# Kernel tuning notes

Measured on AMD Instinct MI355X. Metric: run time of the kernel, lower is better.

Reference implementation:

```python
import jax, jax.numpy as jnp
import numpy as np
from jax import lax

GN_GROUPS = 32
EPS = 1e-5


def conv_gn_silu(x, W, b, scale, bias, stride, padding):
    # Conv2d (OIHW weights, NCHW data) -> GroupNorm(32) -> SiLU
    y = lax.conv_general_dilated(
        x, W, (stride, stride), [(padding, padding), (padding, padding)],
        dimension_numbers=("NCHW", "OIHW", "NCHW")) + b[None, :, None, None]
    B, C, H, Wd = y.shape
    yr = y.reshape(B, GN_GROUPS, C // GN_GROUPS, H, Wd)
    mu = yr.mean(axis=(2, 3, 4), keepdims=True)
    var = yr.var(axis=(2, 3, 4), keepdims=True)
    yn = ((yr - mu) * lax.rsqrt(var + EPS)).reshape(B, C, H, Wd)
    yn = yn * scale[None, :, None, None] + bias[None, :, None, None]
    return yn * jax.nn.sigmoid(yn)  # SiLU


def setup_inputs() -> dict:
    key = jax.random.key(0)
    ks = jax.random.split(key, 8)
    C = 256
    B, H, W = 8, 64, 64
    f = lambda k, shp, s: jax.random.normal(k, shp, dtype=jnp.float32) * s
    return {
        "x": f(ks[0], (B, C, H, W), 1.0),
        "y": f(ks[1], (B, C, H, W), 1.0),
        "Wq": f(ks[2], (C, C, 3, 3), 0.02),
        "bq": jnp.zeros((C,), jnp.float32),
        "gq_scale": jnp.ones((C,), jnp.float32),
        "gq_bias": jnp.zeros((C,), jnp.float32),
        "Wk": f(ks[3], (C, C, 2, 2), 0.02),
        "bk": jnp.zeros((C,), jnp.float32),
        "gk_scale": jnp.ones((C,), jnp.float32),
        "gk_bias": jnp.zeros((C,), jnp.float32),
        "Wv": f(ks[4], (C, C, 2, 2), 0.02),
        "bv": jnp.zeros((C,), jnp.float32),
        "gv_scale": jnp.ones((C,), jnp.float32),
        "gv_bias": jnp.zeros((C,), jnp.float32),
        "gamma": f(ks[5], (1,), 1.0),
    }


def reference(x, y, Wq, bq, gq_scale, gq_bias, Wk, bk, gk_scale, gk_bias,
              Wv, bv, gv_scale, gv_bias, gamma):
    B, C, H, W = x.shape
    sr = 2
    Cq = C  # in_dim // factor, factor=1
    q = conv_gn_silu(x, Wq, bq, gq_scale, gq_bias, stride=1, padding=1)   # [B,Cq,H,W]
    k = conv_gn_silu(y, Wk, bk, gk_scale, gk_bias, stride=sr, padding=0)  # [B,Cq,H/sr,W/sr]
    v = conv_gn_silu(y, Wv, bv, gv_scale, gv_bias, stride=sr, padding=0)  # [B,C,H/sr,W/sr]
    N = H * W
    M = (H // sr) * (W // sr)
    q = q.reshape(B, Cq, N)   # proj_query (pre-permute)
    k = k.reshape(B, Cq, M)   # proj_key
    v = v.reshape(B, C, M)    # proj_value
    scale = 1.0 / np.sqrt(Cq).astype(np.float32)
    energy = jnp.einsum("bcn,bcm->bnm", q, k) * scale       # [B,N,M]
    attn = jax.nn.softmax(energy, axis=-1)                   # softmax over keys
    out = jnp.einsum("bcm,bnm->bcn", v, attn).reshape(B, C, H, W)
    return gamma * out
```

## Files before the change

kernel.cpp:

```cpp
#include <hip/hip_runtime.h>
#include <hip/hip_bf16.h>
#include <math.h>

#define B_ 8
#define C_ 256
#define H_ 64
#define W_ 64
#define N_ 4096
#define M_ 1024
#define HW_ 4096

typedef __attribute__((ext_vector_type(8))) short short8;
typedef __attribute__((ext_vector_type(4))) float f32x4;

__device__ __forceinline__ unsigned short f2bf(float x) {
    unsigned u = __float_as_uint(x);
    u += 0x7fffu + ((u >> 16) & 1u);
    return (unsigned short)(u >> 16);
}
__device__ __forceinline__ float bf2f(unsigned short h) {
    return __uint_as_float(((unsigned)h) << 16);
}

__device__ __forceinline__ void gl_lds16(const unsigned short* g, unsigned short* l) {
    __builtin_amdgcn_global_load_lds(
        (const __attribute__((address_space(1))) unsigned int*)g,
        (__attribute__((address_space(3))) unsigned int*)l, 16, 0, 0);
}

__global__ __launch_bounds__(256) void split_w_tap(
    const float* __restrict__ Wq, unsigned short* __restrict__ wtH,
    unsigned short* __restrict__ wtL)
{
    int co = blockIdx.x, ci = threadIdx.x;
    const float* wp = Wq + ((size_t)co * 256 + ci) * 9;
    #pragma unroll
    for (int tap = 0; tap < 9; ++tap) {
        float v = wp[tap];
        unsigned short h = f2bf(v), l = f2bf(v - bf2f(h));
        size_t o = ((size_t)tap << 16) + ((size_t)co << 8) + ci;
        wtH[o] = h; wtL[o] = l;
    }
}

__global__ __launch_bounds__(256) void split_w2(
    const float* __restrict__ Wsrc, unsigned short* __restrict__ wH,
    unsigned short* __restrict__ wL)
{
    int co = blockIdx.x, ci = threadIdx.x;
    const float* wp = Wsrc + ((size_t)co * 256 + ci) * 4;
    #pragma unroll
    for (int tap = 0; tap < 4; ++tap) {
        float v = wp[tap];
        unsigned short h = f2bf(v), l = f2bf(v - bf2f(h));
        size_t o = ((size_t)tap << 16) + ((size_t)co << 8) + ci;
        wH[o] = h; wL[o] = l;
    }
}

__global__ __launch_bounds__(256) void split_x_pad(
    const float* __restrict__ x, unsigned short* __restrict__ xpH,
    unsigned short* __restrict__ xpL)
{
    __shared__ float tile[64][65];
    int blk = blockIdx.x;
    int b = blk >> 6, h = blk & 63;
    int t = threadIdx.x;
    const float* xb = x + ((size_t)b << 20) + (size_t)h * 64;
    size_t obase = (((size_t)b * 4356) + (size_t)(h + 1) * 66 + 1) * 256;
    unsigned short* oH = xpH + obase;
    unsigned short* oL = xpL + obase;
    for (int cc = 0; cc < 256; cc += 64) {
        int wi = t & 63, cq = t >> 6;
        #pragma unroll
        for (int r = 0; r < 16; ++r) {
            int cl = cq * 16 + r;
            tile[cl][wi] = xb[((size_t)(cc + cl)) * 4096 + wi];
        }
        __syncthreads();
        int cl = t & 63, wq = t >> 6;
        #pragma unroll
        for (int r = 0; r < 16; ++r) {
            int wwi = wq * 16 + r;
            float v = tile[cl][wwi];
            unsigned short hh = f2bf(v), lo = f2bf(v - bf2f(hh));
            size_t o = (size_t)wwi * 256 + cc + cl;
            oH[o] = hh; oL[o] = lo;
        }
        __syncthreads();
    }
}

__global__ __launch_bounds__(256) void split_y_t(
    const float* __restrict__ y, unsigned short* __restrict__ yTh,
    unsigned short* __restrict__ yTl, int b0)
{
    __shared__ float tile[64][65];
    int blk = blockIdx.x;
    int bl = blk >> 6, h = blk & 63;
    int t = threadIdx.x;
    const float* yb = y + ((size_t)(b0 + bl) << 20) + (size_t)h * 64;
    size_t obase = (((size_t)bl << 12) + (size_t)h * 64) * 256;
    unsigned short* oH = yTh + obase;
    unsigned short* oL = yTl + obase;
    for (int cc = 0; cc < 256; cc += 64) {
        int wi = t & 63, cq = t >> 6;
        #pragma unroll
        for (int r = 0; r < 16; ++r) {
            int cl = cq * 16 + r;
            tile[cl][wi] = yb[((size_t)(cc + cl)) * 4096 + wi];
        }
        __syncthreads();
        int cl = t & 63, wq = t >> 6;
        #pragma unroll
        for (int r = 0; r < 16; ++r) {
            int wwi = wq * 16 + r;
            float v = tile[cl][wwi];
            unsigned short hh = f2bf(v), lo = f2bf(v - bf2f(hh));
            size_t o = (size_t)wwi * 256 + cc + cl;
            oH[o] = hh; oL[o] = lo;
        }
        __syncthreads();
    }
}

__global__ __launch_bounds__(256, 2) void conv3x3_mfma(
    const unsigned short* __restrict__ xpH, const unsigned short* __restrict__ xpL,
    const unsigned short* __restrict__ wtH, const unsigned short* __restrict__ wtL,
    const float* __restrict__ bq,
    unsigned short* __restrict__ qH, unsigned short* __restrict__ qL)
{
    __shared__ __align__(16) unsigned short bldsH[272 * 32];
    __shared__ __align__(16) unsigned short bldsL[272 * 32];
    __shared__ __align__(16) unsigned short aldsH[2][128 * 32];
    __shared__ __align__(16) unsigned short aldsL[2][128 * 32];

    int blk = blockIdx.x;
    int bat = blk & 7;
    int rest = blk >> 3;
    int cot = rest & 1;
    int pxt = rest >> 1;
    int t = threadIdx.x;
    int w = t >> 6;
    int wco = w >> 1, wpx = w & 1;
    int lane = t & 63;
    int ll = lane & 15, qd = lane >> 4;
    const int h0 = pxt * 2;
    const int co0b = cot * 128;

    const unsigned short* xpHb = xpH + (size_t)bat * 4356 * 256;
    const unsigned short* xpLb = xpL + (size_t)bat * 4356 * 256;

    f32x4 acc[4][4];
    #pragma unroll
    for (int i = 0; i < 4; ++i)
        #pragma unroll
        for (int j = 0; j < 4; ++j) acc[i][j] = (f32x4){0.f, 0.f, 0.f, 0.f};

    int buf = 0;
    for (int chunk = 0; chunk < 8; ++chunk) {
        const int ci0 = chunk * 32;
        for (int j = w; j < 34; j += 4) {
            int half = (j >= 17);
            int jj = half ? j - 17 : j;
            int gid = jj * 64 + lane;
            int cell = gid >> 2;
            int g = gid & 3;
            int cellc = cell < 264 ? cell : 263;
            int dr = cellc / 66;
            int cc = cellc - dr * 66;
            const unsigned short* src = (half ? xpLb : xpHb)
                + (((size_t)(h0 + dr) * 66 + cc) << 8) + ci0
                + ((g ^ (cellc & 3)) << 3);
            unsigned short* dst = (half ? bldsL : bldsH) + jj * 512;
            gl_lds16(src, dst);
        }
        for (int j = w; j < 16; j += 4) {
            int half = j >> 3;
            int jj = j & 7;
            int gid = jj * 64 + lane;
            int co = gid >> 2;
            int g = gid & 3;
            const unsigned short* src = (half ? wtL : wtH)
                + (((size_t)(co0b + co)) << 8) + ci0 + ((g ^ (co & 3)) << 3);
            unsigned short* dst = (half ? aldsL[buf] : aldsH[buf]) + jj * 512;
            gl_lds16(src, dst);
        }
        __syncthreads();

        for (int tap = 0; tap < 9; ++tap) {
            if (tap < 8) {
                const int aoff = (tap + 1) << 16;
                for (int j = w; j < 16; j += 4) {
                    int half = j >> 3;
                    int jj = j & 7;
                    int gid = jj * 64 + lane;
                    int co = gid >> 2;
                    int g = gid & 3;
                    const unsigned short* src = (half ? wtL : wtH)
                        + aoff + (((size_t)(co0b + co)) << 8) + ci0
                        + ((g ^ (co & 3)) << 3);
                    unsigned short* dst = (half ? aldsL[buf ^ 1] : aldsH[buf ^ 1]) + jj * 512;
                    gl_lds16(src, dst);
                }
            }
            int kh = tap / 3, kw = tap - kh * 3;
            short8 avh[4], avl[4], bvh[4], bvl[4];
            #pragma unroll
            for (int ib = 0; ib < 4; ++ib) {
                int col = wco * 64 + ib * 16 + ll;
                int aa = col * 32 + ((qd ^ (col & 3)) << 3);
                avh[ib] = *(const short8*)&aldsH[buf][aa];
                avl[ib] = *(const short8*)&aldsL[buf][aa];
            }
            #pragma unroll
            for (int jb = 0; jb < 4; ++jb) {
                int cell = (wpx + kh) * 66 + jb * 16 + ll + kw;
                int ba = cell * 32 + ((qd ^ (cell & 3)) << 3);
                bvh[jb] = *(const short8*)&bldsH[ba];
                bvl[jb] = *(const short8*)&bldsL[ba];
            }
            __builtin_amdgcn_s_setprio(1);
            #pragma unroll
            for (int ib = 0; ib < 4; ++ib)
                #pragma unroll
                for (int jb = 0; jb < 4; ++jb) {
                    f32x4 o = acc[ib][jb];
                    o = __builtin_amdgcn_mfma_f32_16x16x32_bf16(avh[ib], bvh[jb], o, 0, 0, 0);
                    o = __builtin_amdgcn_mfma_f32_16x16x32_bf16(avl[ib], bvh[jb], o, 0, 0, 0);
                    o = __builtin_amdgcn_mfma_f32_16x16x32_bf16(avh[ib], bvl[jb], o, 0, 0, 0);
                    acc[ib][jb] = o;
                }
            __builtin_amdgcn_s_setprio(0);
            __syncthreads();
            buf ^= 1;
        }
    }

    const int co0 = cot * 128 + wco * 64;
    const int pxbase = pxt * 128 + wpx * 64;
    #pragma unroll
    for (int ib = 0; ib < 4; ++ib) {
        #pragma unroll
        for (int r = 0; r < 4; ++r) {
            int co = co0 + ib * 16 + qd * 4 + r;
            float bvv = bq[co];
            size_t rowo = ((size_t)(bat * 256 + co)) << 12;
            #pragma unroll
            for (int jb = 0; jb < 4; ++jb) {
                float v = acc[ib][jb][r] + bvv;
                unsigned short h = f2bf(v), l = f2bf(v - bf2f(h));
                size_t o = rowo + pxbase + jb * 16 + ll;
                qH[o] = h; qL[o] = l;
            }
        }
    }
}

__global__ __launch_bounds__(256, 2) void conv2x2_mfma(
    const unsigned short* __restrict__ yTh, const unsigned short* __restrict__ yTl,
    const unsigned short* __restrict__ wkH, const unsigned short* __restrict__ wkL,
    const unsigned short* __restrict__ wvH, const unsigned short* __restrict__ wvL,
    const float* __restrict__ bk, const float* __restrict__ bv,
    float* __restrict__ kf, float* __restrict__ vf, int b0)
{
    int blk = blockIdx.x;
    int batl = blk & 3;
    int sel = (blk >> 2) & 3;
    int mt  = blk >> 4;
    int t = threadIdx.x;
    int wv_ = t >> 6;
    int wco = wv_ >> 1, wpx = wv_ & 1;
    int lane = t & 63;
    int ll = lane & 15, qd = lane >> 4;

    const unsigned short* wtH_; const unsigned short* wtL_;
    const float* bias; float* dst; int co0;
    if (sel < 2) { wtH_ = wkH; wtL_ = wkL; bias = bk; dst = kf; co0 = sel * 128 + wco * 64; }
    else         { wtH_ = wvH; wtL_ = wvL; bias = bv; dst = vf; co0 = (sel - 2) * 128 + wco * 64; }

    const unsigned short* aHp[4]; const unsigned short* aLp[4];
    #pragma unroll
    for (int ib = 0; ib < 4; ++ib) {
        size_t o = ((size_t)(co0 + ib * 16 + ll)) * 256 + qd * 8;
        aHp[ib] = wtH_ + o; aLp[ib] = wtL_ + o;
    }
    const unsigned short* bHp[4]; const unsigned short* bLp[4];
    #pragma unroll
    for (int jb = 0; jb < 4; ++jb) {
        int m = mt * 128 + wpx * 64 + jb * 16 + ll;
        int mh = m >> 5, mw = m & 31;
        size_t o = (((size_t)batl << 12) + (size_t)(2 * mh) * 64 + 2 * mw) * 256 + qd * 8;
        bHp[jb] = yTh + o; bLp[jb] = yTl + o;
    }

    f32x4 acc[4][4];
    #pragma unroll
    for (int i = 0; i < 4; ++i)
        #pragma unroll
        for (int j = 0; j < 4; ++j) acc[i][j] = (f32x4){0.f, 0.f, 0.f, 0.f};

    #pragma unroll
    for (int tap = 0; tap < 4; ++tap) {
        const int aoff = tap << 16;
        const int boff = (((tap >> 1) * 64) + (tap & 1)) * 256;
        #pragma unroll 2
        for (int ci0 = 0; ci0 < 256; ci0 += 32) {
            short8 avh[4], avl[4], bvh[4], bvl[4];
            #pragma unroll
            for (int ib = 0; ib < 4; ++ib) {
                avh[ib] = *(const short8*)(aHp[ib] + aoff + ci0);
                avl[ib] = *(const short8*)(aLp[ib] + aoff + ci0);
            }
            #pragma unroll
            for (int jb = 0; jb < 4; ++jb) {
                bvh[jb] = *(const short8*)(bHp[jb] + boff + ci0);
                bvl[jb] = *(const short8*)(bLp[jb] + boff + ci0);
            }
            #pragma unroll
            for (int ib = 0; ib < 4; ++ib)
                #pragma unroll
                for (int jb = 0; jb < 4; ++jb) {
                    f32x4 o = acc[ib][jb];
                    o = __builtin_amdgcn_mfma_f32_16x16x32_bf16(avh[ib], bvh[jb], o, 0, 0, 0);
                    o = __builtin_amdgcn_mfma_f32_16x16x32_bf16(avl[ib], bvh[jb], o, 0, 0, 0);
                    o = __builtin_amdgcn_mfma_f32_16x16x32_bf16(avh[ib], bvl[jb], o, 0, 0, 0);
                    acc[ib][jb] = o;
                }
        }
    }

    const int mbase = mt * 128 + wpx * 64;
    #pragma unroll
    for (int ib = 0; ib < 4; ++ib) {
        #pragma unroll
        for (int r = 0; r < 4; ++r) {
            int co = co0 + ib * 16 + qd * 4 + r;
            float bvv = bias[co];
            float* op = dst + (((size_t)((b0 + batl) * 256 + co)) << 10) + mbase + ll;
            #pragma unroll
            for (int jb = 0; jb < 4; ++jb)
                op[jb * 16] = acc[ib][jb][r] + bvv;
        }
    }
}

__global__ __launch_bounds__(256) void gn_stats_kernel(
    const float* __restrict__ buf, float* __restrict__ stats, int S)
{
    int bg = blockIdx.x;
    const float4* p = (const float4*)(buf + (size_t)bg * 8 * S);
    int n4 = 2 * S;
    float s = 0.f, s2 = 0.f;
    for (int i = threadIdx.x; i < n4; i += 256) {
        float4 vv = p[i];
        s  += vv.x + vv.y + vv.z + vv.w;
        s2 += vv.x * vv.x + vv.y * vv.y + vv.z * vv.z + vv.w * vv.w;
    }
    for (int d = 1; d < 64; d <<= 1) { s += __shfl_xor(s, d); s2 += __shfl_xor(s2, d); }
    __shared__ float red[8];
    int w = threadIdx.x >> 6;
    if ((threadIdx.x & 63) == 0) { red[w] = s; red[w + 4] = s2; }
    __syncthreads();
    if (threadIdx.x == 0) {
        s  = red[0] + red[1] + red[2] + red[3];
        s2 = red[4] + red[5] + red[6] + red[7];
        float invn = 1.f / (float)(8 * S);
        float mean = s * invn;
        float var = s2 * invn - mean * mean;
        if (var < 0.f) var = 0.f;
        stats[bg * 2]     = mean;
        stats[bg * 2 + 1] = 1.f / sqrtf(var + 1e-5f);
    }
}

__global__ __launch_bounds__(256) void gn_stats_pair(
    const unsigned short* __restrict__ hi, const unsigned short* __restrict__ lo,
    float* __restrict__ stats, int S)
{
    int bg = blockIdx.x;
    const uint4* ph = (const uint4*)(hi + (size_t)bg * 8 * S);
    const uint4* pl = (const uint4*)(lo + (size_t)bg * 8 * S);
    int n8 = S;
    float s = 0.f, s2 = 0.f;
    for (int i = threadIdx.x; i < n8; i += 256) {
        uint4 a = ph[i], b2 = pl[i];
        unsigned ua[4] = {a.x, a.y, a.z, a.w}, ub[4] = {b2.x, b2.y, b2.z, b2.w};
        #pragma unroll
        for (int j = 0; j < 4; ++j) {
            float x0 = __uint_as_float(ua[j] << 16) + __uint_as_float(ub[j] << 16);
            float x1 = __uint_as_float(ua[j] & 0xffff0000u) + __uint_as_float(ub[j] & 0xffff0000u);
            s += x0 + x1;
            s2 += x0 * x0 + x1 * x1;
        }
    }
    for (int d = 1; d < 64; d <<= 1) { s += __shfl_xor(s, d); s2 += __shfl_xor(s2, d); }
    __shared__ float red[8];
    int w = threadIdx.x >> 6;
    if ((threadIdx.x & 63) == 0) { red[w] = s; red[w + 4] = s2; }
    __syncthreads();
    if (threadIdx.x == 0) {
        s  = red[0] + red[1] + red[2] + red[3];
        s2 = red[4] + red[5] + red[6] + red[7];
        float invn = 1.f / (float)(8 * S);
        float mean = s * invn;
        float var = s2 * invn - mean * mean;
        if (var < 0.f) var = 0.f;
        stats[bg * 2]     = mean;
        stats[bg * 2 + 1] = 1.f / sqrtf(var + 1e-5f);
    }
}

__global__ __launch_bounds__(256) void gn_silu_pair(
    unsigned short* __restrict__ hi, unsigned short* __restrict__ lo,
    const float* __restrict__ stats, const float* __restrict__ scale,
    const float* __restrict__ bias, float extra, int total8)
{
    int idx = blockIdx.x * 256 + threadIdx.x;
    if (idx >= total8) return;
    size_t e = (size_t)idx * 8;
    int c  = (int)((e >> 12) & 255);
    int gg = (int)(e >> 15);
    float mean = stats[gg * 2], rstd = stats[gg * 2 + 1];
    float a  = scale[c] * rstd;
    float bb = bias[c] - mean * a;
    uint4 uh = ((uint4*)hi)[idx], ul = ((uint4*)lo)[idx];
    unsigned ha[4] = {uh.x, uh.y, uh.z, uh.w}, la[4] = {ul.x, ul.y, ul.z, ul.w};
    unsigned oh[4], ol[4];
    #pragma unroll
    for (int j = 0; j < 4; ++j) {
        float x0 = __uint_as_float(ha[j] << 16) + __uint_as_float(la[j] << 16);
        float x1 = __uint_as_float(ha[j] & 0xffff0000u) + __uint_as_float(la[j] & 0xffff0000u);
        float y0 = x0 * a + bb, y1 = x1 * a + bb;
        float s0 = extra * y0 / (1.f + __expf(-y0));
        float s1 = extra * y1 / (1.f + __expf(-y1));
        unsigned short h0 = f2bf(s0), l0 = f2bf(s0 - bf2f(h0));
        unsigned short h1 = f2bf(s1), l1 = f2bf(s1 - bf2f(h1));
        oh[j] = h0 | ((unsigned)h1 << 16);
        ol[j] = l0 | ((unsigned)l1 << 16);
    }
    ((uint4*)hi)[idx] = make_uint4(oh[0], oh[1], oh[2], oh[3]);
    ((uint4*)lo)[idx] = make_uint4(ol[0], ol[1], ol[2], ol[3]);
}

__global__ __launch_bounds__(256) void gn_silu_split_v(
    const float* __restrict__ vf, unsigned short* __restrict__ hi,
    unsigned short* __restrict__ lo, const float* __restrict__ stats,
    const float* __restrict__ scale, const float* __restrict__ bias, int total8)
{
    int idx = blockIdx.x * 256 + threadIdx.x;
    if (idx >= total8) return;
    size_t e = (size_t)idx * 8;
    int c  = (int)((e >> 10) & 255);
    int gg = (int)(e >> 13);
    float mean = stats[gg * 2], rstd = stats[gg * 2 + 1];
    float a  = scale[c] * rstd;
    float bb = bias[c] - mean * a;
    float4 f0 = ((const float4*)vf)[idx * 2];
    float4 f1 = ((const float4*)vf)[idx * 2 + 1];
    float xs[8] = {f0.x, f0.y, f0.z, f0.w, f1.x, f1.y, f1.z, f1.w};
    unsigned oh[4], ol[4];
    #pragma unroll
    for (int j = 0; j < 4; ++j) {
        float y0 = xs[2 * j] * a + bb, y1 = xs[2 * j + 1] * a + bb;
        float s0 = y0 / (1.f + __expf(-y0));
        float s1 = y1 / (1.f + __expf(-y1));
        unsigned short h0 = f2bf(s0), l0 = f2bf(s0 - bf2f(h0));
        unsigned short h1 = f2bf(s1), l1 = f2bf(s1 - bf2f(h1));
        oh[j] = h0 | ((unsigned)h1 << 16);
        ol[j] = l0 | ((unsigned)l1 << 16);
    }
    ((uint4*)hi)[idx] = make_uint4(oh[0], oh[1], oh[2], oh[3]);
    ((uint4*)lo)[idx] = make_uint4(ol[0], ol[1], ol[2], ol[3]);
}

__global__ __launch_bounds__(256) void gn_silu_split_kT(
    const float* __restrict__ kf, unsigned short* __restrict__ th,
    unsigned short* __restrict__ tl, const float* __restrict__ stats,
    const float* __restrict__ scale, const float* __restrict__ bias)
{
    int bm = blockIdx.x;
    int b = bm >> 7, m8 = (bm & 127) * 8;
    int c = threadIdx.x;
    int gg = b * 32 + (c >> 3);
    float mean = stats[gg * 2], rstd = stats[gg * 2 + 1];
    float a  = scale[c] * rstd;
    float bb = bias[c] - mean * a;
    const float* src = kf + (((size_t)(b * 256 + c)) << 10) + m8;
    float4 f0 = *(const float4*)src;
    float4 f1 = *(const float4*)(src + 4);
    float xs[8] = {f0.x, f0.y, f0.z, f0.w, f1.x, f1.y, f1.z, f1.w};
    #pragma unroll
    for (int j = 0; j < 8; ++j) {
        float y = xs[j] * a + bb;
        float s = y / (1.f + __expf(-y));
        unsigned short h = f2bf(s), l = f2bf(s - bf2f(h));
        size_t o = ((size_t)b * M_ + m8 + j) * C_ + c;
        th[o] = h;
        tl[o] = l;
    }
}

__global__ __launch_bounds__(256, 2) void attn_mfma(
    const unsigned short* __restrict__ qh, const unsigned short* __restrict__ qlo,
    const unsigned short* __restrict__ kth, const unsigned short* __restrict__ ktl,
    const unsigned short* __restrict__ vh, const unsigned short* __restrict__ vlo,
    const float* __restrict__ gamma, float* __restrict__ out)
{
    __shared__ __align__(16) unsigned short kldsH[32 * 256];
    __shared__ __align__(16) unsigned short kldsL[32 * 256];
    __shared__ __align__(16) unsigned short vldsH[256 * 32];
    __shared__ __align__(16) unsigned short vldsL[256 * 32];
    __shared__ __align__(16) unsigned short pH[4][16][40];
    __shared__ __align__(16) unsigned short pL[4][16][40];
    __shared__ float alphaS[4][16];

    int blk = blockIdx.x;
    int bat = blk & 7;
    int nt  = blk >> 3;
    int t = threadIdx.x;
    int w = t >> 6;
    int lane = t & 63;
    int ll = lane & 15;
    int qd = lane >> 4;
    int n0 = nt * 64 + w * 16;

    short8 aqh[8], aql[8];
    {
        const unsigned short* qb1 = qh  + (size_t)bat * C_ * N_ + n0 + ll;
        const unsigned short* qb2 = qlo + (size_t)bat * C_ * N_ + n0 + ll;
        #pragma unroll
        for (int ks = 0; ks < 8; ++ks) {
            #pragma unroll
            for (int j = 0; j < 8; ++j) {
                size_t off = (size_t)(ks * 32 + qd * 8 + j) * N_;
                aqh[ks][j] = (short)qb1[off];
                aql[ks][j] = (short)qb2[off];
            }
        }
    }

    f32x4 oacc[16];
    #pragma unroll
    for (int i = 0; i < 16; ++i) oacc[i] = (f32x4){0.f, 0.f, 0.f, 0.f};
    f32x4 lacc = (f32x4){0.f, 0.f, 0.f, 0.f};
    float mrun[4] = {-3e38f, -3e38f, -3e38f, -3e38f};
    const short8 ones = (short8){16256, 16256, 16256, 16256, 16256, 16256, 16256, 16256};

    const unsigned short* kg = ((w & 1) == 0 ? kth : ktl) + (size_t)bat * M_ * C_;
    const unsigned short* vg = ((w & 1) == 0 ? vh  : vlo) + (size_t)bat * C_ * M_;
    unsigned short* kdst = (w & 1) ? kldsL : kldsH;
    unsigned short* vdst = (w & 1) ? vldsL : vldsH;
    const int krow  = lane >> 5;
    const int kcolg = lane & 31;
    const int vc_l  = lane >> 2;
    const int vg_g  = lane & 3;

    for (int mt = 0; mt < 32; ++mt) {
        const int m0 = mt * 32;
        if (w < 2) {
            #pragma unroll
            for (int i = 0; i < 16; ++i) {
                int row = 2 * i + krow;
                const unsigned short* src = kg + (size_t)(m0 + row) * 256
                                            + ((kcolg ^ (row & 7)) << 3);
                gl_lds16(src, kdst + i * 512);
            }
        } else {
            #pragma unroll
            for (int i = 0; i < 16; ++i) {
                int c = i * 16 + vc_l;
                const unsigned short* src = vg + (size_t)c * M_ + m0
                                            + ((vg_g ^ (c & 3)) << 3);
                gl_lds16(src, vdst + i * 512);
            }
        }
        __syncthreads();

        f32x4 s0 = {0.f, 0.f, 0.f, 0.f}, s1 = {0.f, 0.f, 0.f, 0.f};
        __builtin_amdgcn_s_setprio(1);
        #pragma unroll
        for (int ks = 0; ks < 8; ++ks) {
            int cg = ks * 4 + qd;
            int a0 = ll * 256 + ((cg ^ (ll & 7)) << 3);
            int a1 = (ll + 16) * 256 + ((cg ^ (ll & 7)) << 3);
            short8 b0h = *(const short8*)&kldsH[a0];
            short8 b1h = *(const short8*)&kldsH[a1];
            short8 b0l = *(const short8*)&kldsL[a0];
            short8 b1l = *(const short8*)&kldsL[a1];
            s0 = __builtin_amdgcn_mfma_f32_16x16x32_bf16(aqh[ks], b0h, s0, 0, 0, 0);
            s1 = __builtin_amdgcn_mfma_f32_16x16x32_bf16(aqh[ks], b1h, s1, 0, 0, 0);
            s0 = __builtin_amdgcn_mfma_f32_16x16x32_bf16(aql[ks], b0h, s0, 0, 0, 0);
            s1 = __builtin_amdgcn_mfma_f32_16x16x32_bf16(aql[ks], b1h, s1, 0, 0, 0);
            s0 = __builtin_amdgcn_mfma_f32_16x16x32_bf16(aqh[ks], b0l, s0, 0, 0, 0);
            s1 = __builtin_amdgcn_mfma_f32_16x16x32_bf16(aqh[ks], b1l, s1, 0, 0, 0);
        }
        __builtin_amdgcn_s_setprio(0);

        float alpha4[4];
        #pragma unroll
        for (int r = 0; r < 4; ++r) {
            float mx = fmaxf(s0[r], s1[r]);
            mx = fmaxf(mx, __shfl_xor(mx, 1));
            mx = fmaxf(mx, __shfl_xor(mx, 2));
            mx = fmaxf(mx, __shfl_xor(mx, 4));
            mx = fmaxf(mx, __shfl_xor(mx, 8));
            float mn = fmaxf(mrun[r], mx);
            float al = __expf(mrun[r] - mn);
            mrun[r] = mn;
            float p0 = __expf(s0[r] - mn);
            float p1 = __expf(s1[r] - mn);
            alpha4[r] = al;
            unsigned short h0 = f2bf(p0), l0 = f2bf(p0 - bf2f(h0));
            unsigned short h1 = f2bf(p1), l1 = f2bf(p1 - bf2f(h1));
            int rn = qd * 4 + r;
            pH[w][rn][ll] = h0;  pH[w][rn][16 + ll] = h1;
            pL[w][rn][ll] = l0;  pL[w][rn][16 + ll] = l1;
        }
        if (ll == 0) {
            #pragma unroll
            for (int r = 0; r < 4; ++r) alphaS[w][qd * 4 + r] = alpha4[r];
        }
        __builtin_amdgcn_wave_barrier();
        short8 bph = *(const short8*)&pH[w][ll][qd * 8];
        short8 bpl = *(const short8*)&pL[w][ll][qd * 8];
        float an = alphaS[w][ll];
        {
            f32x4 o = lacc;
            o[0] *= an; o[1] *= an; o[2] *= an; o[3] *= an;
            o = __builtin_amdgcn_mfma_f32_16x16x32_bf16(ones, bph, o, 0, 0, 0);
            o = __builtin_amdgcn_mfma_f32_16x16x32_bf16(ones, bpl, o, 0, 0, 0);
            lacc = o;
        }
        __builtin_amdgcn_s_setprio(1);
        #pragma unroll
        for (int ct = 0; ct < 16; ++ct) {
            int c = ct * 16 + ll;
            int av = c * 32 + ((qd ^ (c & 3)) << 3);
            short8 avh = *(const short8*)&vldsH[av];
            short8 avl = *(const short8*)&vldsL[av];
            f32x4 o = oacc[ct];
            o[0] *= an; o[1] *= an; o[2] *= an; o[3] *= an;
            o = __builtin_amdgcn_mfma_f32_16x16x32_bf16(avh, bph, o, 0, 0, 0);
            o = __builtin_amdgcn_mfma_f32_16x16x32_bf16(avl, bph, o, 0, 0, 0);
            o = __builtin_amdgcn_mfma_f32_16x16x32_bf16(avh, bpl, o, 0, 0, 0);
            oacc[ct] = o;
        }
        __builtin_amdgcn_s_setprio(0);
        __syncthreads();
    }

    float linv = gamma[0] / lacc[0];
    float* ob = out + (size_t)bat * C_ * N_ + n0 + ll;
    #pragma unroll
    for (int ct = 0; ct < 16; ++ct) {
        #pragma unroll
        for (int r = 0; r < 4; ++r) {
            int c = ct * 16 + qd * 4 + r;
            ob[(size_t)c * N_] = oacc[ct][r] * linv;
        }
    }
}

extern "C" void kernel_launch(void* const* d_in, const int* in_sizes, int n_in,
                              void* d_out, int out_size, void* d_ws, size_t ws_size,
                              hipStream_t stream)
{
    const float* x   = (const float*)d_in[0];
    const float* y   = (const float*)d_in[1];
    const float* Wq  = (const float*)d_in[2];
    const float* bq  = (const float*)d_in[3];
    const float* gqs = (const float*)d_in[4];
    const float* gqb = (const float*)d_in[5];
    const float* Wk  = (const float*)d_in[6];
    const float* bk  = (const float*)d_in[7];
    const float* gks = (const float*)d_in[8];
    const float* gkb = (const float*)d_in[9];
    const float* Wv  = (const float*)d_in[10];
    const float* bv  = (const float*)d_in[11];
    const float* gvs = (const float*)d_in[12];
    const float* gvb = (const float*)d_in[13];
    const float* gamma = (const float*)d_in[14];
    float* out = (float*)d_out;

    char* base = (char*)d_ws;
    unsigned short* qH = (unsigned short*)base;
    unsigned short* qL = qH + 8388608;
    char* regA = (char*)(qL + 8388608);
    unsigned short* xpH = (unsigned short*)regA;
    unsigned short* xpL = xpH + 8921088;
    unsigned short* wtH = xpL + 8921088;
    unsigned short* wtL = wtH + 589824;
    float* kf = (float*)regA;
    float* vf = kf + 2097152;
    unsigned short* kTh = (unsigned short*)(vf + 2097152);
    unsigned short* kTl = kTh + 2097152;
    unsigned short* vH  = kTl + 2097152;
    unsigned short* vL  = vH + 2097152;
    float* stq = (float*)(vL + 2097152);
    float* stk = stq + 512;
    float* stv = stk + 512;
    unsigned short* yTh  = (unsigned short*)(vf + 2097152);
    unsigned short* yTl  = yTh + 4194304;
    unsigned short* w2kH = yTl + 4194304;
    unsigned short* w2kL = w2kH + 262144;
    unsigned short* w2vH = w2kL + 262144;
    unsigned short* w2vL = w2vH + 262144;

    hipMemsetAsync(xpH, 0, (size_t)2 * 8921088 * sizeof(unsigned short), stream);
    split_w_tap<<<256, 256, 0, stream>>>(Wq, wtH, wtL);
    split_x_pad<<<512, 256, 0, stream>>>(x, xpH, xpL);
    conv3x3_mfma<<<512, 256, 0, stream>>>(xpH, xpL, wtH, wtL, bq, qH, qL);

    split_w2<<<256, 256, 0, stream>>>(Wk, w2kH, w2kL);
    split_w2<<<256, 256, 0, stream>>>(Wv, w2vH, w2vL);
    split_y_t<<<256, 256, 0, stream>>>(y, yTh, yTl, 0);
    conv2x2_mfma<<<128, 256, 0, stream>>>(yTh, yTl, w2kH, w2kL, w2vH, w2vL,
                                          bk, bv, kf, vf, 0);
    split_y_t<<<256, 256, 0, stream>>>(y, yTh, yTl, 4);
    conv2x2_mfma<<<128, 256, 0, stream>>>(yTh, yTl, w2kH, w2kL, w2vH, w2vL,
                                          bk, bv, kf, vf, 4);

    gn_stats_pair<<<256, 256, 0, stream>>>(qH, qL, stq, 4096);
    gn_stats_kernel<<<256, 256, 0, stream>>>(kf, stk, 1024);
    gn_stats_kernel<<<256, 256, 0, stream>>>(vf, stv, 1024);
    gn_silu_pair<<<4096, 256, 0, stream>>>(qH, qL, stq, gqs, gqb, 0.0625f, 1048576);
    gn_silu_split_v<<<1024, 256, 0, stream>>>(vf, vH, vL, stv, gvs, gvb, 262144);
    gn_silu_split_kT<<<1024, 256, 0, stream>>>(kf, kTh, kTl, stk, gks, gkb);
    attn_mfma<<<512, 256, 0, stream>>>(qH, qL, kTh, kTl, vH, vL, gamma, out);
}
```

Before: 559.5 us.

## Stage conv2x2 input tiles in LDS and fuse q GroupNorm-SiLU into attention

The 2x2 stride-2 conv now stages each 32-channel slice of the input rows into swizzled LDS once per block and reads all four taps from LDS, instead of fetching B operands straight from global memory per tap. The separate q GroupNorm+SiLU elementwise pass is removed: the stats kernel emits per-channel affine coefficients and the attention kernel applies normalize, SiLU and the hi/lo split while loading Q. This saves a full read-write pass over q at the cost of extra math in the attention prologue. The V LDS swizzle pattern is also changed to reduce bank conflicts.

```diff
diff --git a/kernel.cpp b/kernel.cpp
--- a/kernel.cpp
+++ b/kernel.cpp
@@ -264,13 +264,16 @@
     const float* __restrict__ bk, const float* __restrict__ bv,
     float* __restrict__ kf, float* __restrict__ vf, int b0)
 {
+    __shared__ __align__(16) unsigned short bldsH[512 * 32];
+    __shared__ __align__(16) unsigned short bldsL[512 * 32];
+
     int blk = blockIdx.x;
     int batl = blk & 3;
     int sel = (blk >> 2) & 3;
     int mt  = blk >> 4;
     int t = threadIdx.x;
-    int wv_ = t >> 6;
-    int wco = wv_ >> 1, wpx = wv_ & 1;
+    int w = t >> 6;
+    int wco = w >> 1, wpx = w & 1;
     int lane = t & 63;
     int ll = lane & 15, qd = lane >> 4;
 
@@ -285,14 +288,14 @@
         size_t o = ((size_t)(co0 + ib * 16 + ll)) * 256 + qd * 8;
         aHp[ib] = wtH_ + o; aLp[ib] = wtL_ + o;
     }
-    const unsigned short* bHp[4]; const unsigned short* bLp[4];
-    #pragma unroll
-    for (int jb = 0; jb < 4; ++jb) {
-        int m = mt * 128 + wpx * 64 + jb * 16 + ll;
-        int mh = m >> 5, mw = m & 31;
-        size_t o = (((size_t)batl << 12) + (size_t)(2 * mh) * 64 + 2 * mw) * 256 + qd * 8;
-        bHp[jb] = yTh + o; bLp[jb] = yTl + o;
-    }
+    const unsigned short* ySH = yTh + ((((size_t)batl << 12) + mt * 512) << 8);
+    const unsigned short* ySL = yTl + ((((size_t)batl << 12) + mt * 512) << 8);
+    const int half_ = w >> 1;
+    const int gi0 = (w & 1) * 16;
+    const unsigned short* yS = half_ ? ySL : ySH;
+    unsigned short* bd = half_ ? bldsL : bldsH;
+    const int scell = lane >> 2;
+    const int sg = lane & 3;
 
     f32x4 acc[4][4];
     #pragma unroll
@@ -300,23 +303,37 @@
         #pragma unroll
         for (int j = 0; j < 4; ++j) acc[i][j] = (f32x4){0.f, 0.f, 0.f, 0.f};
 
-    #pragma unroll
-    for (int tap = 0; tap < 4; ++tap) {
-        const int aoff = tap << 16;
-        const int boff = (((tap >> 1) * 64) + (tap & 1)) * 256;
-        #pragma unroll 2
-        for (int ci0 = 0; ci0 < 256; ci0 += 32) {
+    for (int chunk = 0; chunk < 8; ++chunk) {
+        const int ci0 = chunk * 32;
+        #pragma unroll
+        for (int j = 0; j < 16; ++j) {
+            int gi = gi0 + j;
+            int cell = gi * 16 + scell;
+            const unsigned short* src = yS + ((size_t)cell << 8) + ci0
+                                        + ((sg ^ ((cell >> 1) & 3)) << 3);
+            gl_lds16(src, bd + gi * 512);
+        }
+        __syncthreads();
+
+        #pragma unroll
+        for (int tap = 0; tap < 4; ++tap) {
+            int kh = tap >> 1, kw = tap & 1;
+            const int aoff = (tap << 16) + ci0;
             short8 avh[4], avl[4], bvh[4], bvl[4];
             #pragma unroll
             for (int ib = 0; ib < 4; ++ib) {
-                avh[ib] = *(const short8*)(aHp[ib] + aoff + ci0);
-                avl[ib] = *(const short8*)(aLp[ib] + aoff + ci0);
+                avh[ib] = *(const short8*)(aHp[ib] + aoff);
+                avl[ib] = *(const short8*)(aLp[ib] + aoff);
             }
             #pragma unroll
             for (int jb = 0; jb < 4; ++jb) {
-                bvh[jb] = *(const short8*)(bHp[jb] + boff + ci0);
-                bvl[jb] = *(const short8*)(bLp[jb] + boff + ci0);
-            }
+                int mlocal = wpx * 64 + jb * 16 + ll;
+                int cell = (2 * (mlocal >> 5) + kh) * 64 + 2 * (mlocal & 31) + kw;
+                int ba = cell * 32 + ((qd ^ ((cell >> 1) & 3)) << 3);
+                bvh[jb] = *(const short8*)&bldsH[ba];
+                bvl[jb] = *(const short8*)&bldsL[ba];
+            }
+            __builtin_amdgcn_s_setprio(1);
             #pragma unroll
             for (int ib = 0; ib < 4; ++ib)
                 #pragma unroll
@@ -327,7 +344,9 @@
                     o = __builtin_amdgcn_mfma_f32_16x16x32_bf16(avh[ib], bvl[jb], o, 0, 0, 0);
                     acc[ib][jb] = o;
                 }
-        }
+            __builtin_amdgcn_s_setprio(0);
+        }
+        __syncthreads();
     }
 
     const int mbase = mt * 128 + wpx * 64;
@@ -376,7 +395,8 @@
 
 __global__ __launch_bounds__(256) void gn_stats_pair(
     const unsigned short* __restrict__ hi, const unsigned short* __restrict__ lo,
-    float* __restrict__ stats, int S)
+    const float* __restrict__ scale, const float* __restrict__ bias,
+    float2* __restrict__ ab, int S)
 {
     int bg = blockIdx.x;
     const uint4* ph = (const uint4*)(hi + (size_t)bg * 8 * S);
@@ -396,6 +416,7 @@
     }
     for (int d = 1; d < 64; d <<= 1) { s += __shfl_xor(s, d); s2 += __shfl_xor(s2, d); }
     __shared__ float red[8];
+    __shared__ float mv[2];
     int w = threadIdx.x >> 6;
     if ((threadIdx.x & 63) == 0) { red[w] = s; red[w + 4] = s2; }
     __syncthreads();
@@ -406,41 +427,16 @@
         float mean = s * invn;
         float var = s2 * invn - mean * mean;
         if (var < 0.f) var = 0.f;
-        stats[bg * 2]     = mean;
-        stats[bg * 2 + 1] = 1.f / sqrtf(var + 1e-5f);
-    }
-}
-
-__global__ __launch_bounds__(256) void gn_silu_pair(
-    unsigned short* __restrict__ hi, unsigned short* __restrict__ lo,
-    const float* __restrict__ stats, const float* __restrict__ scale,
-    const float* __restrict__ bias, float extra, int total8)
-{
-    int idx = blockIdx.x * 256 + threadIdx.x;
-    if (idx >= total8) return;
-    size_t e = (size_t)idx * 8;
-    int c  = (int)((e >> 12) & 255);
-    int gg = (int)(e >> 15);
-    float mean = stats[gg * 2], rstd = stats[gg * 2 + 1];
-    float a  = scale[c] * rstd;
-    float bb = bias[c] - mean * a;
-    uint4 uh = ((uint4*)hi)[idx], ul = ((uint4*)lo)[idx];
-    unsigned ha[4] = {uh.x, uh.y, uh.z, uh.w}, la[4] = {ul.x, ul.y, ul.z, ul.w};
-    unsigned oh[4], ol[4];
-    #pragma unroll
-    for (int j = 0; j < 4; ++j) {
-        float x0 = __uint_as_float(ha[j] << 16) + __uint_as_float(la[j] << 16);
-        float x1 = __uint_as_float(ha[j] & 0xffff0000u) + __uint_as_float(la[j] & 0xffff0000u);
-        float y0 = x0 * a + bb, y1 = x1 * a + bb;
-        float s0 = extra * y0 / (1.f + __expf(-y0));
-        float s1 = extra * y1 / (1.f + __expf(-y1));
-        unsigned short h0 = f2bf(s0), l0 = f2bf(s0 - bf2f(h0));
-        unsigned short h1 = f2bf(s1), l1 = f2bf(s1 - bf2f(h1));
-        oh[j] = h0 | ((unsigned)h1 << 16);
-        ol[j] = l0 | ((unsigned)l1 << 16);
-    }
-    ((uint4*)hi)[idx] = make_uint4(oh[0], oh[1], oh[2], oh[3]);
-    ((uint4*)lo)[idx] = make_uint4(ol[0], ol[1], ol[2], ol[3]);
+        mv[0] = mean;
+        mv[1] = 1.f / sqrtf(var + 1e-5f);
+    }
+    __syncthreads();
+    if (threadIdx.x < 8) {
+        int c = (bg & 31) * 8 + threadIdx.x;
+        float a = scale[c] * mv[1];
+        float bb = bias[c] - mv[0] * a;
+        ab[(bg >> 5) * 256 + c] = make_float2(a, bb);
+    }
 }
 
 __global__ __launch_bounds__(256) void gn_silu_split_v(
@@ -505,6 +501,7 @@
     const unsigned short* __restrict__ qh, const unsigned short* __restrict__ qlo,
     const unsigned short* __restrict__ kth, const unsigned short* __restrict__ ktl,
     const unsigned short* __restrict__ vh, const unsigned short* __restrict__ vlo,
+    const float2* __restrict__ abq,
     const float* __restrict__ gamma, float* __restrict__ out)
 {
     __shared__ __align__(16) unsigned short kldsH[32 * 256];
@@ -529,13 +526,20 @@
     {
         const unsigned short* qb1 = qh  + (size_t)bat * C_ * N_ + n0 + ll;
         const unsigned short* qb2 = qlo + (size_t)bat * C_ * N_ + n0 + ll;
+        const float2* ab = abq + bat * 256;
         #pragma unroll
         for (int ks = 0; ks < 8; ++ks) {
             #pragma unroll
             for (int j = 0; j < 8; ++j) {
-                size_t off = (size_t)(ks * 32 + qd * 8 + j) * N_;
-                aqh[ks][j] = (short)qb1[off];
-                aql[ks][j] = (short)qb2[off];
+                int c = ks * 32 + qd * 8 + j;
+                size_t off = (size_t)c * N_;
+                float xv = bf2f(qb1[off]) + bf2f(qb2[off]);
+                float2 t2 = ab[c];
+                float yv = xv * t2.x + t2.y;
+                float sv = 0.0625f * yv / (1.f + __expf(-yv));
+                unsigned short h = f2bf(sv);
+                aqh[ks][j] = (short)h;
+                aql[ks][j] = (short)f2bf(sv - bf2f(h));
             }
         }
     }
@@ -571,7 +575,7 @@
             for (int i = 0; i < 16; ++i) {
                 int c = i * 16 + vc_l;
                 const unsigned short* src = vg + (size_t)c * M_ + m0
-                                            + ((vg_g ^ (c & 3)) << 3);
+                                            + ((vg_g ^ ((c >> 1) & 3)) << 3);
                 gl_lds16(src, vdst + i * 512);
             }
         }
@@ -636,7 +640,7 @@
         #pragma unroll
         for (int ct = 0; ct < 16; ++ct) {
             int c = ct * 16 + ll;
-            int av = c * 32 + ((qd ^ (c & 3)) << 3);
+            int av = c * 32 + ((qd ^ ((c >> 1) & 3)) << 3);
             short8 avh = *(const short8*)&vldsH[av];
             short8 avl = *(const short8*)&vldsL[av];
             f32x4 o = oacc[ct];
@@ -700,6 +704,7 @@
     float* stq = (float*)(vL + 2097152);
     float* stk = stq + 512;
     float* stv = stk + 512;
+    float2* abq = (float2*)(stv + 512);
     unsigned short* yTh  = (unsigned short*)(vf + 2097152);
     unsigned short* yTl  = yTh + 4194304;
     unsigned short* w2kH = yTl + 4194304;
@@ -721,11 +726,10 @@
     conv2x2_mfma<<<128, 256, 0, stream>>>(yTh, yTl, w2kH, w2kL, w2vH, w2vL,
                                           bk, bv, kf, vf, 4);
 
-    gn_stats_pair<<<256, 256, 0, stream>>>(qH, qL, stq, 4096);
+    gn_stats_pair<<<256, 256, 0, stream>>>(qH, qL, gqs, gqb, abq, 4096);
     gn_stats_kernel<<<256, 256, 0, stream>>>(kf, stk, 1024);
     gn_stats_kernel<<<256, 256, 0, stream>>>(vf, stv, 1024);
-    gn_silu_pair<<<4096, 256, 0, stream>>>(qH, qL, stq, gqs, gqb, 0.0625f, 1048576);
     gn_silu_split_v<<<1024, 256, 0, stream>>>(vf, vH, vL, stv, gvs, gvb, 262144);
     gn_silu_split_kT<<<1024, 256, 0, stream>>>(kf, kTh, kTl, stk, gks, gkb);
-    attn_mfma<<<512, 256, 0, stream>>>(qH, qL, kTh, kTl, vH, vL, gamma, out);
-}
+    attn_mfma<<<512, 256, 0, stream>>>(qH, qL, kTh, kTl, vH, vL, abq, gamma, out);
+}
```

Result: faster. 505.8 us (-9.6%).
